# Performance work log

Hardware: AMD Instinct MI355X
Metric: run time of the kernel (lower is better)

The kernel has to match this reference:

```python
import jax, jax.numpy as jnp
import numpy as np

N_NODES = 30000
NEG_SLOPE = 0.2  # PyG GATConv default leaky_relu slope


def gat_conv(x, src, dst, W, a_src, a_dst, b, num_nodes, concat):
    """One PyG-style GATConv layer (add_self_loops already applied to src/dst).
    x: [N, F_in]; W: [F_in, H*C]; a_src, a_dst: [H, C]; b: [H*C] or [C].
    """
    H, C = a_src.shape
    h = (x @ W).reshape(num_nodes, H, C)                     # [N, H, C]
    alpha_src = jnp.einsum('nhc,hc->nh', h, a_src)           # [N, H]
    alpha_dst = jnp.einsum('nhc,hc->nh', h, a_dst)           # [N, H]
    e = jax.nn.leaky_relu(alpha_src[src] + alpha_dst[dst], NEG_SLOPE)  # [E, H]
    # scatter-softmax over incoming edges of each dst node
    e_max = jax.ops.segment_max(e, dst, num_segments=num_nodes)        # [N, H]
    e_exp = jnp.exp(e - e_max[dst])                                    # [E, H]
    denom = jax.ops.segment_sum(e_exp, dst, num_segments=num_nodes)    # [N, H]
    alpha = e_exp / denom[dst]                                         # [E, H]
    msg = h[src] * alpha[:, :, None]                                   # [E, H, C]
    out = jax.ops.segment_sum(msg, dst, num_segments=num_nodes)        # [N, H, C]
    out = out.reshape(num_nodes, H * C) if concat else out.mean(axis=1)
    return out + b


def _glorot(key, shape):
    fan = sum(shape[:2]) if len(shape) > 1 else shape[0] * 2
    return jax.random.normal(key, shape, dtype=jnp.float32) * np.sqrt(2.0 / fan)


def setup_inputs() -> dict:
    key = jax.random.key(0)
    ks = jax.random.split(key, 16)
    n, f_in, heads = N_NODES, 256, 4
    x = jax.random.normal(ks[0], (n, f_in), dtype=jnp.float32)
    edge_index = jax.random.randint(ks[1], (2, 480000), 0, n, dtype=jnp.int64)
    inp = {
        'x': x, 'edge_index': edge_index,
        'W1': _glorot(ks[2], (f_in, heads * 128)),
        'a1s': _glorot(ks[3], (heads, 128)), 'a1d': _glorot(ks[4], (heads, 128)),
        'b1': jnp.zeros((heads * 128,), jnp.float32),
        'W2': _glorot(ks[5], (heads * 128, heads * 128)),
        'a2s': _glorot(ks[6], (heads, 128)), 'a2d': _glorot(ks[7], (heads, 128)),
        'b2': jnp.zeros((heads * 128,), jnp.float32),
        'W3': _glorot(ks[8], (heads * 128, heads * 64)),
        'a3s': _glorot(ks[9], (heads, 64)), 'a3d': _glorot(ks[10], (heads, 64)),
        'b3': jnp.zeros((heads * 64,), jnp.float32),
        # conv4: 256 -> 64, 1 head, mean (concat=False)
        'W4': _glorot(ks[11], (heads * 64, 64)),
        'a4s': _glorot(ks[12], (1, 64)), 'a4d': _glorot(ks[13], (1, 64)),
        'b4': jnp.zeros((64,), jnp.float32),
    }
    return inp


def reference(x, edge_index, W1, a1s, a1d, b1, W2, a2s, a2d, b2,
              W3, a3s, a3d, b3, W4, a4s, a4d, b4):
    n = x.shape[0]
    # PyG GATConv default add_self_loops=True
    loops = jnp.arange(n, dtype=edge_index.dtype)
    src = jnp.concatenate([edge_index[0], loops])
    dst = jnp.concatenate([edge_index[1], loops])
    h = jax.nn.relu(gat_conv(x, src, dst, W1, a1s, a1d, b1, n, True))
    h = jax.nn.relu(gat_conv(h, src, dst, W2, a2s, a2d, b2, n, True))
    h = jax.nn.relu(gat_conv(h, src, dst, W3, a3s, a3d, b3, n, True))
    h = jax.nn.relu(gat_conv(h, src, dst, W4, a4s, a4d, b4, n, False))
    return h
```

## Files before the change

### kernel.cpp

```cpp
#include <hip/hip_runtime.h>
#include <hip/hip_fp16.h>
#include <math.h>


typedef __attribute__((ext_vector_type(8))) __bf16 bf16x8;
typedef __attribute__((ext_vector_type(4))) float floatx4;
typedef __attribute__((ext_vector_type(8))) unsigned short usv8;
typedef __attribute__((ext_vector_type(4))) unsigned short usv4;

#define DEG_CAP 256

__device__ __forceinline__ unsigned short f2bf(float f) {
    unsigned int u = __float_as_uint(f);
    u += 0x7fff + ((u >> 16) & 1);
    return (unsigned short)(u >> 16);
}
__device__ __forceinline__ float bf2f(unsigned short u) {
    return __uint_as_float(((unsigned int)u) << 16);
}
__device__ __forceinline__ float lrelu(float e) {
    return (e > 0.f) ? e : 0.2f * e;
}
__device__ __forceinline__ void gload16(const void* g, void* l) {
    __builtin_amdgcn_global_load_lds(
        (const __attribute__((address_space(1))) void*)g,
        (__attribute__((address_space(3))) void*)l, 16, 0, 0);
}

static __global__ void zero_float(float* __restrict__ p, int n) {
    int i = blockIdx.x * blockDim.x + threadIdx.x;
    if (i < n) p[i] = 0.f;
}
static __global__ void zero_int(int* __restrict__ p, int n) {
    int i = blockIdx.x * blockDim.x + threadIdx.x;
    if (i < n) p[i] = 0;
}

static __global__ void hist_kernel(const int* __restrict__ ei, int e0, int n_nodes,
                                   int* __restrict__ counts) {
    int e = blockIdx.x * blockDim.x + threadIdx.x;
    int et = e0 + n_nodes;
    if (e >= et) return;
    int d = (e < e0) ? ei[e0 + e] : (e - e0);
    atomicAdd(&counts[d], 1);
}

static __global__ void scan_kernel(const int* __restrict__ counts,
                                   int* __restrict__ row_ptr,
                                   int* __restrict__ cursor, int n) {
    __shared__ int sdata[1024];
    int tid = threadIdx.x;
    int per = (n + 1023) / 1024;
    int start = tid * per;
    int stop = min(start + per, n);
    if (start > n) start = n;
    int s = 0;
    for (int i = start; i < stop; i++) s += counts[i];
    sdata[tid] = s;
    __syncthreads();
    for (int off = 1; off < 1024; off <<= 1) {
        int t = (tid >= off) ? sdata[tid - off] : 0;
        __syncthreads();
        sdata[tid] += t;
        __syncthreads();
    }
    int run = sdata[tid] - s;
    for (int i = start; i < stop; i++) {
        row_ptr[i] = run;
        cursor[i] = run;
        run += counts[i];
    }
    if (stop == n) row_ptr[n] = run;
}

static __global__ void scatter_kernel(const int* __restrict__ ei, int e0, int n_nodes,
                                      int* __restrict__ cursor,
                                      int* __restrict__ src_sorted) {
    int e = blockIdx.x * blockDim.x + threadIdx.x;
    int et = e0 + n_nodes;
    if (e >= et) return;
    int s, d;
    if (e < e0) { s = ei[e]; d = ei[e0 + e]; } else { s = e - e0; d = s; }
    int pos = atomicAdd(&cursor[d], 1);
    src_sorted[pos] = s;
}

static __global__ void convA_kernel(const float* __restrict__ X,
                                    unsigned short* __restrict__ A, int M, int K) {
    int idx = blockIdx.x * 256 + threadIdx.x;
    if (idx >= M * K) return;
    int m = idx / K, k = idx % K;
    float v = X[idx];
    unsigned short hi = f2bf(v);
    size_t base = (size_t)m * (2 * K);
    A[base + k] = hi;
    A[base + K + k] = f2bf(v - bf2f(hi));
}

__device__ __forceinline__ void convW_one(const float* W, unsigned short* BT,
                                          int idx, int K, int N) {
    int n = idx / K, k = idx % K;
    float v = (n < N) ? W[(size_t)k * N + n] : 0.f;
    unsigned short hi = f2bf(v);
    size_t base = (size_t)n * (2 * K);
    BT[base + k] = hi;
    BT[base + K + k] = f2bf(v - bf2f(hi));
}

static __global__ void convW_all(const float* __restrict__ W1, unsigned short* __restrict__ BT1,
                                 const float* __restrict__ W2, unsigned short* __restrict__ BT2,
                                 const float* __restrict__ W3, unsigned short* __restrict__ BT3,
                                 const float* __restrict__ W4, unsigned short* __restrict__ BT4) {
    int idx = blockIdx.x * 256 + threadIdx.x;
    if (idx < 131072) { convW_one(W1, BT1, idx, 256, 512); return; }
    idx -= 131072;
    if (idx < 262144) { convW_one(W2, BT2, idx, 512, 512); return; }
    idx -= 262144;
    if (idx < 131072) { convW_one(W3, BT3, idx, 512, 256); return; }
    idx -= 131072;
    if (idx < 32768)  { convW_one(W4, BT4, idx, 256, 64); }
}

#define BM 128
#define BN 128
#define BKK 32

__launch_bounds__(256, 3)
static __global__ void gemm_mfma(const unsigned short* __restrict__ A,
                                 const unsigned short* __restrict__ B,
                                 __half* __restrict__ C, int M, int K, int N,
                                 int xcols, int mblocks,
                                 const float* __restrict__ asv,
                                 const float* __restrict__ adv,
                                 float* __restrict__ as_out,
                                 float* __restrict__ ad_out,
                                 int Hh, int Cc) {
    __shared__ __align__(16) unsigned short lds[4 * BM * BKK];
    const int tid  = threadIdx.x;
    const int lane = tid & 63;
    const int wave = tid >> 6;

    const int id = blockIdx.x;
    const int band = id / (8 * xcols);
    const int rem = id - band * 8 * xcols;
    const int band_rows = min(8, mblocks - band * 8);
    const int ry = rem % band_rows;
    const int rx = rem / band_rows;
    const int r0 = (band * 8 + ry) * BM;
    const int c0 = rx * BN;

    const int wm = (wave >> 1) * 64;
    const int wn = (wave & 1) * 64;
    const int q   = lane >> 4;
    const int m16 = lane & 15;

    floatx4 acc[4][4];
#pragma unroll
    for (int i = 0; i < 4; i++)
#pragma unroll
        for (int j = 0; j < 4; j++) acc[i][j] = {0.f, 0.f, 0.f, 0.f};

    const size_t sA = (size_t)(2 * K);
    const size_t sB = (size_t)(2 * K);
    char* ldsb = (char*)lds;

#pragma unroll 1
    for (int k0 = 0; k0 < K; k0 += BKK) {
        __syncthreads();
#pragma unroll
        for (int c = 0; c < 2; c++) {
            int slot = c * 256 + tid;
            int row = slot >> 2;
            int gc  = (slot & 3) ^ ((row >> 1) & 3);
            const unsigned short* Ab = A + (size_t)(r0 + row) * sA + k0 + gc * 8;
            const unsigned short* Bb = B + (size_t)(c0 + row) * sB + k0 + gc * 8;
            gload16(Ab,     ldsb + slot * 16);
            gload16(Ab + K, ldsb + 8192 + slot * 16);
            gload16(Bb,     ldsb + 16384 + slot * 16);
            gload16(Bb + K, ldsb + 24576 + slot * 16);
        }
        __syncthreads();
        bf16x8 ah[4], al[4], bh[4], bl[4];
#pragma unroll
        for (int i = 0; i < 4; i++) {
            int row = wm + i * 16 + m16;
            int ch  = q ^ ((row >> 1) & 3);
            int off = (row * 4 + ch) * 16;
            ah[i] = *(const bf16x8*)(ldsb + off);
            al[i] = *(const bf16x8*)(ldsb + 8192 + off);
        }
#pragma unroll
        for (int j = 0; j < 4; j++) {
            int row = wn + j * 16 + m16;
            int ch  = q ^ ((row >> 1) & 3);
            int off = (row * 4 + ch) * 16;
            bh[j] = *(const bf16x8*)(ldsb + 16384 + off);
            bl[j] = *(const bf16x8*)(ldsb + 24576 + off);
        }
#pragma unroll
        for (int i = 0; i < 4; i++)
#pragma unroll
            for (int j = 0; j < 4; j++) {
                acc[i][j] = __builtin_amdgcn_mfma_f32_16x16x32_bf16(
                    ah[i], bh[j], acc[i][j], 0, 0, 0);
                acc[i][j] = __builtin_amdgcn_mfma_f32_16x16x32_bf16(
                    al[i], bh[j], acc[i][j], 0, 0, 0);
                acc[i][j] = __builtin_amdgcn_mfma_f32_16x16x32_bf16(
                    ah[i], bl[j], acc[i][j], 0, 0, 0);
            }
    }
#pragma unroll
    for (int i = 0; i < 4; i++)
#pragma unroll
        for (int j = 0; j < 4; j++)
#pragma unroll
            for (int r = 0; r < 4; r++) {
                int row = r0 + wm + i * 16 + q * 4 + r;
                int col = c0 + wn + j * 16 + m16;
                if (row < M && col < N)
                    C[(size_t)row * N + col] = __float2half(acc[i][j][r]);
            }
    if (c0 + wn < N) {
        int head = (c0 + wn) / Cc;
#pragma unroll
        for (int i = 0; i < 4; i++)
#pragma unroll
            for (int r = 0; r < 4; r++) {
                float ps = 0.f, pd = 0.f;
#pragma unroll
                for (int j = 0; j < 4; j++) {
                    int c = c0 + wn + j * 16 + m16;
                    float v = acc[i][j][r];
                    ps = fmaf(v, asv[c], ps);
                    pd = fmaf(v, adv[c], pd);
                }
#pragma unroll
                for (int off = 1; off < 16; off <<= 1) {
                    ps += __shfl_xor(ps, off);
                    pd += __shfl_xor(pd, off);
                }
                if (m16 == 0) {
                    int row = r0 + wm + i * 16 + q * 4 + r;
                    if (row < M) {
                        atomicAdd(&as_out[(size_t)row * Hh + head], ps);
                        atomicAdd(&ad_out[(size_t)row * Hh + head], pd);
                    }
                }
            }
    }
}

template <int R>
__device__ __forceinline__ void accum_row(const __half* hptr, size_t off, float w,
                                          float* acc) {
    const __half* p = hptr + off;
    if constexpr (R == 8) {
        float4 raw = *(const float4*)p;
        const __half* hv = (const __half*)&raw;
#pragma unroll
        for (int r = 0; r < 8; r++) acc[r] = fmaf(__half2float(hv[r]), w, acc[r]);
    } else if constexpr (R == 4) {
        float2 raw = *(const float2*)p;
        const __half* hv = (const __half*)&raw;
#pragma unroll
        for (int r = 0; r < 4; r++) acc[r] = fmaf(__half2float(hv[r]), w, acc[r]);
    } else {
        acc[0] = fmaf(__half2float(*p), w, acc[0]);
    }
}

template <int H, int C, bool BF16OUT>
__launch_bounds__(256)
static __global__ void agg_kernel(const __half* __restrict__ h,
                                  const float* __restrict__ as_arr,
                                  const float* __restrict__ ad_arr,
                                  const int* __restrict__ row_ptr,
                                  const int* __restrict__ src_sorted,
                                  const float* __restrict__ bias,
                                  float* __restrict__ outf,
                                  unsigned short* __restrict__ outb,
                                  float* __restrict__ znext_as,
                                  float* __restrict__ znext_ad, int n_nodes) {
    constexpr int R = H * C / 64;
    constexpr int G = 64 / H;
    constexpr int K = H * C;
    __shared__ float lds_e[4][DEG_CAP * H];
    __shared__ int   lds_s[4][DEG_CAP];
    int wave = threadIdx.x >> 6;
    int lane = threadIdx.x & 63;
    int n = blockIdx.x * 4 + wave;
    if (n >= n_nodes) return;
    int beg = row_ptr[n], end = row_ptr[n + 1];
    float* we = lds_e[wave];
    int*   ls = lds_s[wave];

    float ad_h[H], m_h[H], l_h[H];
#pragma unroll
    for (int hh = 0; hh < H; hh++) {
        ad_h[hh] = ad_arr[(size_t)n * H + hh];
        m_h[hh] = -INFINITY;
        l_h[hh] = 0.f;
    }
    for (int base = beg; base < end; base += 64) {
        int j = base + lane;
        bool ok = j < end;
        float e_h[H];
        if (ok) {
            int s = src_sorted[j];
            if constexpr (H == 4) {
                float4 a = ((const float4*)as_arr)[s];
                e_h[0] = lrelu(a.x + ad_h[0]);
                e_h[1] = lrelu(a.y + ad_h[1]);
                e_h[2] = lrelu(a.z + ad_h[2]);
                e_h[3] = lrelu(a.w + ad_h[3]);
            } else {
                e_h[0] = lrelu(as_arr[s] + ad_h[0]);
            }
            int idx = j - beg;
            if (idx < DEG_CAP) {
                ls[idx] = s;
                if constexpr (H == 4) {
                    *(float4*)&we[idx * 4] = make_float4(e_h[0], e_h[1], e_h[2], e_h[3]);
                } else {
                    we[idx] = e_h[0];
                }
            }
        } else {
#pragma unroll
            for (int hh = 0; hh < H; hh++) e_h[hh] = -INFINITY;
        }
#pragma unroll
        for (int hh = 0; hh < H; hh++) {
            float cm = e_h[hh];
#pragma unroll
            for (int off = 1; off < 64; off <<= 1) cm = fmaxf(cm, __shfl_xor(cm, off));
            float newm = fmaxf(m_h[hh], cm);
            float p = ok ? __expf(e_h[hh] - newm) : 0.f;
#pragma unroll
            for (int off = 1; off < 64; off <<= 1) p += __shfl_xor(p, off);
            l_h[hh] = l_h[hh] * __expf(m_h[hh] - newm) + p;
            m_h[hh] = newm;
        }
    }
    int myh = lane / G;
    float mm, adm, inv;
    if constexpr (H == 4) {
        mm  = m_h[0];  mm  = (myh == 1) ? m_h[1] : mm;  mm  = (myh == 2) ? m_h[2] : mm;  mm  = (myh == 3) ? m_h[3] : mm;
        float ll = l_h[0]; ll = (myh == 1) ? l_h[1] : ll; ll = (myh == 2) ? l_h[2] : ll; ll = (myh == 3) ? l_h[3] : ll;
        adm = ad_h[0]; adm = (myh == 1) ? ad_h[1] : adm; adm = (myh == 2) ? ad_h[2] : adm; adm = (myh == 3) ? ad_h[3] : adm;
        inv = 1.f / ll;
    } else {
        mm = m_h[0]; adm = ad_h[0]; inv = 1.f / l_h[0];
    }

    float acc[R];
#pragma unroll
    for (int r = 0; r < R; r++) acc[r] = 0.f;

    int j = beg;
    for (; j + 7 < end; j += 8) {
        int i0 = j - beg;
        int ss[8];
        float ee[8];
        if (i0 + 7 < DEG_CAP) {
#pragma unroll
            for (int u = 0; u < 8; u++) {
                ss[u] = ls[i0 + u];
                ee[u] = we[(i0 + u) * H + myh];
            }
        } else {
#pragma unroll
            for (int u = 0; u < 8; u++) {
                ss[u] = src_sorted[j + u];
                ee[u] = lrelu(as_arr[(size_t)ss[u] * H + myh] + adm);
            }
        }
        float ww[8];
#pragma unroll
        for (int u = 0; u < 8; u++) ww[u] = __expf(ee[u] - mm) * inv;
#pragma unroll
        for (int u = 0; u < 8; u++)
            accum_row<R>(h, (size_t)ss[u] * K + lane * R, ww[u], acc);
    }
    for (; j < end; j++) {
        int i0 = j - beg;
        int s0;
        float e0;
        if (i0 < DEG_CAP) {
            s0 = ls[i0];
            e0 = we[i0 * H + myh];
        } else {
            s0 = src_sorted[j];
            e0 = lrelu(as_arr[(size_t)s0 * H + myh] + adm);
        }
        float w0 = __expf(e0 - mm) * inv;
        accum_row<R>(h, (size_t)s0 * K + lane * R, w0, acc);
    }

    if (znext_as != nullptr && lane == 0) {
        if constexpr (H == 4) {
            *(float4*)&znext_as[(size_t)n * 4] = make_float4(0.f, 0.f, 0.f, 0.f);
            *(float4*)&znext_ad[(size_t)n * 4] = make_float4(0.f, 0.f, 0.f, 0.f);
        } else {
            znext_as[n] = 0.f;
            znext_ad[n] = 0.f;
        }
    }
    float vout[R];
#pragma unroll
    for (int r = 0; r < R; r++)
        vout[r] = fmaxf(acc[r] + bias[lane * R + r], 0.f);

    if constexpr (BF16OUT) {
        unsigned short hi[R], lo[R];
#pragma unroll
        for (int r = 0; r < R; r++) {
            hi[r] = f2bf(vout[r]);
            lo[r] = f2bf(vout[r] - bf2f(hi[r]));
        }
        size_t base = (size_t)n * (2 * K) + lane * R;
        if constexpr (R == 8) {
            usv8 vh = {hi[0], hi[1], hi[2], hi[3], hi[4], hi[5], hi[6], hi[7]};
            usv8 vl = {lo[0], lo[1], lo[2], lo[3], lo[4], lo[5], lo[6], lo[7]};
            *(usv8*)(outb + base) = vh;
            *(usv8*)(outb + base + K) = vl;
        } else if constexpr (R == 4) {
            usv4 vh = {hi[0], hi[1], hi[2], hi[3]};
            usv4 vl = {lo[0], lo[1], lo[2], lo[3]};
            *(usv4*)(outb + base) = vh;
            *(usv4*)(outb + base + K) = vl;
        } else {
#pragma unroll
            for (int r = 0; r < R; r++) {
                outb[base + r] = hi[r];
                outb[base + K + r] = lo[r];
            }
        }
    } else {
#pragma unroll
        for (int r = 0; r < R; r++)
            outf[(size_t)n * K + lane * R + r] = vout[r];
    }
}


static inline size_t align_up(size_t x) { return (x + 255) & ~(size_t)255; }

extern "C" void kernel_launch(void* const* d_in, const int* in_sizes, int n_in,
                              void* d_out, int out_size, void* d_ws, size_t ws_size,
                              hipStream_t stream) {
    const float* x   = (const float*)d_in[0];
    const int*   ei  = (const int*)d_in[1];
    const float* W1  = (const float*)d_in[2];
    const float* a1s = (const float*)d_in[3];
    const float* a1d = (const float*)d_in[4];
    const float* b1  = (const float*)d_in[5];
    const float* W2  = (const float*)d_in[6];
    const float* a2s = (const float*)d_in[7];
    const float* a2d = (const float*)d_in[8];
    const float* b2  = (const float*)d_in[9];
    const float* W3  = (const float*)d_in[10];
    const float* a3s = (const float*)d_in[11];
    const float* a3d = (const float*)d_in[12];
    const float* b3  = (const float*)d_in[13];
    const float* W4  = (const float*)d_in[14];
    const float* a4s = (const float*)d_in[15];
    const float* a4d = (const float*)d_in[16];
    const float* b4  = (const float*)d_in[17];

    const int n  = in_sizes[0] / 256;
    const int e0 = in_sizes[1] / 2;
    const int et = e0 + n;
    const int Mpad = ((n + 127) / 128) * 128;

    char* w = (char*)d_ws;
    unsigned short* slotA = (unsigned short*)w;  w += align_up((size_t)Mpad * 1024 * 2);
    __half* hbuf = (__half*)w;                   w += align_up((size_t)n * 512 * 4);
    unsigned short* WT1 = (unsigned short*)w;    w += align_up((size_t)512 * 512 * 2);
    unsigned short* WT2 = (unsigned short*)w;    w += align_up((size_t)512 * 1024 * 2);
    unsigned short* WT3 = (unsigned short*)w;    w += align_up((size_t)256 * 1024 * 2);
    unsigned short* WT4 = (unsigned short*)w;    w += align_up((size_t)128 * 512 * 2);
    float* asA = (float*)w;                      w += align_up((size_t)n * 4 * 4);
    float* adA = (float*)w;                      w += align_up((size_t)n * 4 * 4);
    float* asB = (float*)w;                      w += align_up((size_t)n * 4 * 4);
    float* adB = (float*)w;                      w += align_up((size_t)n * 4 * 4);
    int* row_ptr = (int*)w;                      w += align_up((size_t)(n + 1) * 4);
    int* counts  = (int*)w;                      w += align_up((size_t)n * 4);
    int* cursor  = (int*)w;                      w += align_up((size_t)n * 4);
    int* src_sorted = (int*)w;                   w += align_up((size_t)et * 4);
    (void)ws_size;

    dim3 blk(256);
    int nodeblocks = (n + 3) / 4;

    zero_int<<<(n + 255) / 256, 256, 0, stream>>>(counts, n);
    hist_kernel<<<(et + 255) / 256, 256, 0, stream>>>(ei, e0, n, counts);
    scan_kernel<<<1, 1024, 0, stream>>>(counts, row_ptr, cursor, n);
    scatter_kernel<<<(et + 255) / 256, 256, 0, stream>>>(ei, e0, n, cursor, src_sorted);

    convA_kernel<<<((n * 256) + 255) / 256, blk, 0, stream>>>(x, slotA, n, 256);
    convW_all<<<(557056 + 255) / 256, blk, 0, stream>>>(W1, WT1, W2, WT2, W3, WT3, W4, WT4);
    zero_float<<<(n * 8 + 255) / 256, blk, 0, stream>>>(asA, n * 8);

    const int mblocks = Mpad / 128;

    gemm_mfma<<<dim3(4 * mblocks), blk, 0, stream>>>(slotA, WT1, hbuf, n, 256, 512, 4, mblocks,
                                                     a1s, a1d, asA, adA, 4, 128);
    agg_kernel<4, 128, true><<<nodeblocks, blk, 0, stream>>>(hbuf, asA, adA, row_ptr, src_sorted, b1, nullptr, slotA, asB, adB, n);

    gemm_mfma<<<dim3(4 * mblocks), blk, 0, stream>>>(slotA, WT2, hbuf, n, 512, 512, 4, mblocks,
                                                     a2s, a2d, asB, adB, 4, 128);
    agg_kernel<4, 128, true><<<nodeblocks, blk, 0, stream>>>(hbuf, asB, adB, row_ptr, src_sorted, b2, nullptr, slotA, asA, adA, n);

    gemm_mfma<<<dim3(2 * mblocks), blk, 0, stream>>>(slotA, WT3, hbuf, n, 512, 256, 2, mblocks,
                                                     a3s, a3d, asA, adA, 4, 64);
    agg_kernel<4, 64, true><<<nodeblocks, blk, 0, stream>>>(hbuf, asA, adA, row_ptr, src_sorted, b3, nullptr, slotA, asB, adB, n);

    gemm_mfma<<<dim3(1 * mblocks), blk, 0, stream>>>(slotA, WT4, hbuf, n, 256, 64, 1, mblocks,
                                                     a4s, a4d, asB, adB, 1, 64);
    agg_kernel<1, 64, false><<<nodeblocks, blk, 0, stream>>>(hbuf, asB, adB, row_ptr, src_sorted, b4, (float*)d_out, nullptr, nullptr, nullptr, n);
}
```

Baseline: 646.0 us.

## Split GAT aggregation into edge-weight pass and column-sliced gather kernel

Splits each multi-head aggregation into two kernels. A per-node softmax kernel writes normalized edge weights to a global buffer. A sliced aggregation kernel then assigns each wave one node and a 64-column slice, so many more blocks run in parallel. The goal is more parallelism and lower register pressure in the gather. In exchange it adds kernel launches, a round trip of edge weights through global memory, repeated index reads per slice, and narrower 2-byte gathers instead of 16-byte vector loads. The last layer gets a dedicated single-head kernel.

New measurement: 860.9 us. 1.33x slower.

```diff
diff --git a/kernel.cpp b/kernel.cpp
--- a/kernel.cpp
+++ b/kernel.cpp
@@ -5,8 +5,6 @@
 
 typedef __attribute__((ext_vector_type(8))) __bf16 bf16x8;
 typedef __attribute__((ext_vector_type(4))) float floatx4;
-typedef __attribute__((ext_vector_type(8))) unsigned short usv8;
-typedef __attribute__((ext_vector_type(4))) unsigned short usv4;
 
 #define DEG_CAP 256
 
@@ -250,49 +248,22 @@
     }
 }
 
-template <int R>
-__device__ __forceinline__ void accum_row(const __half* hptr, size_t off, float w,
-                                          float* acc) {
-    const __half* p = hptr + off;
-    if constexpr (R == 8) {
-        float4 raw = *(const float4*)p;
-        const __half* hv = (const __half*)&raw;
-#pragma unroll
-        for (int r = 0; r < 8; r++) acc[r] = fmaf(__half2float(hv[r]), w, acc[r]);
-    } else if constexpr (R == 4) {
-        float2 raw = *(const float2*)p;
-        const __half* hv = (const __half*)&raw;
-#pragma unroll
-        for (int r = 0; r < 4; r++) acc[r] = fmaf(__half2float(hv[r]), w, acc[r]);
-    } else {
-        acc[0] = fmaf(__half2float(*p), w, acc[0]);
-    }
-}
-
-template <int H, int C, bool BF16OUT>
+template <int H>
 __launch_bounds__(256)
-static __global__ void agg_kernel(const __half* __restrict__ h,
-                                  const float* __restrict__ as_arr,
-                                  const float* __restrict__ ad_arr,
-                                  const int* __restrict__ row_ptr,
-                                  const int* __restrict__ src_sorted,
-                                  const float* __restrict__ bias,
-                                  float* __restrict__ outf,
-                                  unsigned short* __restrict__ outb,
-                                  float* __restrict__ znext_as,
-                                  float* __restrict__ znext_ad, int n_nodes) {
-    constexpr int R = H * C / 64;
-    constexpr int G = 64 / H;
-    constexpr int K = H * C;
+static __global__ void weight_kernel(const float* __restrict__ as_arr,
+                                     const float* __restrict__ ad_arr,
+                                     const int* __restrict__ row_ptr,
+                                     const int* __restrict__ src_sorted,
+                                     float* __restrict__ wout, int E_tot,
+                                     float* __restrict__ znext_as,
+                                     float* __restrict__ znext_ad, int n_nodes) {
     __shared__ float lds_e[4][DEG_CAP * H];
-    __shared__ int   lds_s[4][DEG_CAP];
     int wave = threadIdx.x >> 6;
     int lane = threadIdx.x & 63;
     int n = blockIdx.x * 4 + wave;
     if (n >= n_nodes) return;
     int beg = row_ptr[n], end = row_ptr[n + 1];
     float* we = lds_e[wave];
-    int*   ls = lds_s[wave];
 
     float ad_h[H], m_h[H], l_h[H];
 #pragma unroll
@@ -318,7 +289,6 @@
             }
             int idx = j - beg;
             if (idx < DEG_CAP) {
-                ls[idx] = s;
                 if constexpr (H == 4) {
                     *(float4*)&we[idx * 4] = make_float4(e_h[0], e_h[1], e_h[2], e_h[3]);
                 } else {
@@ -342,105 +312,172 @@
             m_h[hh] = newm;
         }
     }
-    int myh = lane / G;
-    float mm, adm, inv;
-    if constexpr (H == 4) {
-        mm  = m_h[0];  mm  = (myh == 1) ? m_h[1] : mm;  mm  = (myh == 2) ? m_h[2] : mm;  mm  = (myh == 3) ? m_h[3] : mm;
-        float ll = l_h[0]; ll = (myh == 1) ? l_h[1] : ll; ll = (myh == 2) ? l_h[2] : ll; ll = (myh == 3) ? l_h[3] : ll;
-        adm = ad_h[0]; adm = (myh == 1) ? ad_h[1] : adm; adm = (myh == 2) ? ad_h[2] : adm; adm = (myh == 3) ? ad_h[3] : adm;
-        inv = 1.f / ll;
-    } else {
-        mm = m_h[0]; adm = ad_h[0]; inv = 1.f / l_h[0];
-    }
-
-    float acc[R];
-#pragma unroll
-    for (int r = 0; r < R; r++) acc[r] = 0.f;
-
+    float inv_h[H];
+#pragma unroll
+    for (int hh = 0; hh < H; hh++) inv_h[hh] = 1.f / l_h[hh];
+
+    if (znext_as != nullptr && lane == 0) {
+        *(float4*)&znext_as[(size_t)n * 4] = make_float4(0.f, 0.f, 0.f, 0.f);
+        *(float4*)&znext_ad[(size_t)n * 4] = make_float4(0.f, 0.f, 0.f, 0.f);
+    }
+
+    for (int base = beg; base < end; base += 64) {
+        int j = base + lane;
+        if (j < end) {
+            int idx = j - beg;
+            float e_h[H];
+            if (idx < DEG_CAP) {
+                if constexpr (H == 4) {
+                    float4 t = *(const float4*)&we[idx * 4];
+                    e_h[0] = t.x; e_h[1] = t.y; e_h[2] = t.z; e_h[3] = t.w;
+                } else {
+                    e_h[0] = we[idx];
+                }
+            } else {
+                int s = src_sorted[j];
+                if constexpr (H == 4) {
+                    float4 a = ((const float4*)as_arr)[s];
+                    e_h[0] = lrelu(a.x + ad_h[0]);
+                    e_h[1] = lrelu(a.y + ad_h[1]);
+                    e_h[2] = lrelu(a.z + ad_h[2]);
+                    e_h[3] = lrelu(a.w + ad_h[3]);
+                } else {
+                    e_h[0] = lrelu(as_arr[s] + ad_h[0]);
+                }
+            }
+#pragma unroll
+            for (int hh = 0; hh < H; hh++)
+                wout[(size_t)hh * E_tot + j] = __expf(e_h[hh] - m_h[hh]) * inv_h[hh];
+        }
+    }
+}
+
+template <int H, int C, bool BF16OUT>
+__launch_bounds__(256)
+static __global__ void slice_agg(const __half* __restrict__ h,
+                                 const float* __restrict__ wbuf,
+                                 const int* __restrict__ row_ptr,
+                                 const int* __restrict__ src_sorted,
+                                 const float* __restrict__ bias,
+                                 float* __restrict__ outf,
+                                 unsigned short* __restrict__ outb,
+                                 int E_tot, int n_nodes) {
+    constexpr int K = H * C;
+    constexpr int NS = K / 64;
+    int id = blockIdx.x;
+    int nb = id / NS;
+    int slice = id - nb * NS;
+    int wave = threadIdx.x >> 6;
+    int lane = threadIdx.x & 63;
+    int n = nb * 4 + wave;
+    if (n >= n_nodes) return;
+    int col = slice * 64 + lane;
+    int head = (slice * 64) / C;
+    const float* wh = wbuf + (size_t)head * E_tot;
+    int beg = row_ptr[n], end = row_ptr[n + 1];
+
+    float acc = 0.f;
     int j = beg;
     for (; j + 7 < end; j += 8) {
+        int ss[8];
+        float wg[8];
+#pragma unroll
+        for (int u = 0; u < 8; u++) ss[u] = src_sorted[j + u];
+#pragma unroll
+        for (int u = 0; u < 8; u++) wg[u] = wh[j + u];
+        __half hv[8];
+#pragma unroll
+        for (int u = 0; u < 8; u++) hv[u] = h[(size_t)ss[u] * K + col];
+#pragma unroll
+        for (int u = 0; u < 8; u++) acc = fmaf(__half2float(hv[u]), wg[u], acc);
+    }
+    for (; j < end; j++) {
+        int s = src_sorted[j];
+        float wg = wh[j];
+        acc = fmaf(__half2float(h[(size_t)s * K + col]), wg, acc);
+    }
+
+    float v = fmaxf(acc + bias[col], 0.f);
+    if constexpr (BF16OUT) {
+        unsigned short hi = f2bf(v);
+        unsigned short lo = f2bf(v - bf2f(hi));
+        size_t base = (size_t)n * (2 * K) + col;
+        outb[base] = hi;
+        outb[base + K] = lo;
+    } else {
+        outf[(size_t)n * K + col] = v;
+    }
+}
+
+__launch_bounds__(256)
+static __global__ void agg4_kernel(const __half* __restrict__ h,
+                                   const float* __restrict__ as_arr,
+                                   const float* __restrict__ ad_arr,
+                                   const int* __restrict__ row_ptr,
+                                   const int* __restrict__ src_sorted,
+                                   const float* __restrict__ bias,
+                                   float* __restrict__ outf, int n_nodes) {
+    __shared__ float lds_e[4][DEG_CAP];
+    int wave = threadIdx.x >> 6;
+    int lane = threadIdx.x & 63;
+    int n = blockIdx.x * 4 + wave;
+    if (n >= n_nodes) return;
+    int beg = row_ptr[n], end = row_ptr[n + 1];
+    float* we = lds_e[wave];
+
+    float ad_n = ad_arr[n];
+    float m = -INFINITY, l = 0.f;
+    for (int base = beg; base < end; base += 64) {
+        int j = base + lane;
+        bool ok = j < end;
+        float e = -INFINITY;
+        if (ok) {
+            int s = src_sorted[j];
+            e = lrelu(as_arr[s] + ad_n);
+            int idx = j - beg;
+            if (idx < DEG_CAP) we[idx] = e;
+        }
+        float cm = e;
+#pragma unroll
+        for (int off = 1; off < 64; off <<= 1) cm = fmaxf(cm, __shfl_xor(cm, off));
+        float newm = fmaxf(m, cm);
+        float p = ok ? __expf(e - newm) : 0.f;
+#pragma unroll
+        for (int off = 1; off < 64; off <<= 1) p += __shfl_xor(p, off);
+        l = l * __expf(m - newm) + p;
+        m = newm;
+    }
+    float inv = 1.f / l;
+
+    float acc = 0.f;
+    int j = beg;
+    for (; j + 3 < end; j += 4) {
         int i0 = j - beg;
-        int ss[8];
-        float ee[8];
-        if (i0 + 7 < DEG_CAP) {
-#pragma unroll
-            for (int u = 0; u < 8; u++) {
-                ss[u] = ls[i0 + u];
-                ee[u] = we[(i0 + u) * H + myh];
-            }
+        int ss[4];
+        float ee[4];
+#pragma unroll
+        for (int u = 0; u < 4; u++) ss[u] = src_sorted[j + u];
+        if (i0 + 3 < DEG_CAP) {
+#pragma unroll
+            for (int u = 0; u < 4; u++) ee[u] = we[i0 + u];
         } else {
 #pragma unroll
-            for (int u = 0; u < 8; u++) {
-                ss[u] = src_sorted[j + u];
-                ee[u] = lrelu(as_arr[(size_t)ss[u] * H + myh] + adm);
-            }
-        }
-        float ww[8];
-#pragma unroll
-        for (int u = 0; u < 8; u++) ww[u] = __expf(ee[u] - mm) * inv;
-#pragma unroll
-        for (int u = 0; u < 8; u++)
-            accum_row<R>(h, (size_t)ss[u] * K + lane * R, ww[u], acc);
+            for (int u = 0; u < 4; u++) ee[u] = lrelu(as_arr[ss[u]] + ad_n);
+        }
+        __half hv[4];
+#pragma unroll
+        for (int u = 0; u < 4; u++) hv[u] = h[(size_t)ss[u] * 64 + lane];
+#pragma unroll
+        for (int u = 0; u < 4; u++)
+            acc = fmaf(__half2float(hv[u]), __expf(ee[u] - m) * inv, acc);
     }
     for (; j < end; j++) {
         int i0 = j - beg;
-        int s0;
-        float e0;
-        if (i0 < DEG_CAP) {
-            s0 = ls[i0];
-            e0 = we[i0 * H + myh];
-        } else {
-            s0 = src_sorted[j];
-            e0 = lrelu(as_arr[(size_t)s0 * H + myh] + adm);
-        }
-        float w0 = __expf(e0 - mm) * inv;
-        accum_row<R>(h, (size_t)s0 * K + lane * R, w0, acc);
-    }
-
-    if (znext_as != nullptr && lane == 0) {
-        if constexpr (H == 4) {
-            *(float4*)&znext_as[(size_t)n * 4] = make_float4(0.f, 0.f, 0.f, 0.f);
-            *(float4*)&znext_ad[(size_t)n * 4] = make_float4(0.f, 0.f, 0.f, 0.f);
-        } else {
-            znext_as[n] = 0.f;
-            znext_ad[n] = 0.f;
-        }
-    }
-    float vout[R];
-#pragma unroll
-    for (int r = 0; r < R; r++)
-        vout[r] = fmaxf(acc[r] + bias[lane * R + r], 0.f);
-
-    if constexpr (BF16OUT) {
-        unsigned short hi[R], lo[R];
-#pragma unroll
-        for (int r = 0; r < R; r++) {
-            hi[r] = f2bf(vout[r]);
-            lo[r] = f2bf(vout[r] - bf2f(hi[r]));
-        }
-        size_t base = (size_t)n * (2 * K) + lane * R;
-        if constexpr (R == 8) {
-            usv8 vh = {hi[0], hi[1], hi[2], hi[3], hi[4], hi[5], hi[6], hi[7]};
-            usv8 vl = {lo[0], lo[1], lo[2], lo[3], lo[4], lo[5], lo[6], lo[7]};
-            *(usv8*)(outb + base) = vh;
-            *(usv8*)(outb + base + K) = vl;
-        } else if constexpr (R == 4) {
-            usv4 vh = {hi[0], hi[1], hi[2], hi[3]};
-            usv4 vl = {lo[0], lo[1], lo[2], lo[3]};
-            *(usv4*)(outb + base) = vh;
-            *(usv4*)(outb + base + K) = vl;
-        } else {
-#pragma unroll
-            for (int r = 0; r < R; r++) {
-                outb[base + r] = hi[r];
-                outb[base + K + r] = lo[r];
-            }
-        }
-    } else {
-#pragma unroll
-        for (int r = 0; r < R; r++)
-            outf[(size_t)n * K + lane * R + r] = vout[r];
-    }
+        int s = src_sorted[j];
+        float e = (i0 < DEG_CAP) ? we[i0] : lrelu(as_arr[s] + ad_n);
+        acc = fmaf(__half2float(h[(size_t)s * 64 + lane]), __expf(e - m) * inv, acc);
+    }
+    outf[(size_t)n * 64 + lane] = fmaxf(acc + bias[lane], 0.f);
 }
 
 
@@ -475,7 +512,8 @@
 
     char* w = (char*)d_ws;
     unsigned short* slotA = (unsigned short*)w;  w += align_up((size_t)Mpad * 1024 * 2);
-    __half* hbuf = (__half*)w;                   w += align_up((size_t)n * 512 * 4);
+    __half* hbuf = (__half*)w;                   w += align_up((size_t)n * 512 * 2);
+    float* wbuf = (float*)w;                     w += align_up((size_t)4 * et * 4);
     unsigned short* WT1 = (unsigned short*)w;    w += align_up((size_t)512 * 512 * 2);
     unsigned short* WT2 = (unsigned short*)w;    w += align_up((size_t)512 * 1024 * 2);
     unsigned short* WT3 = (unsigned short*)w;    w += align_up((size_t)256 * 1024 * 2);
@@ -506,17 +544,20 @@
 
     gemm_mfma<<<dim3(4 * mblocks), blk, 0, stream>>>(slotA, WT1, hbuf, n, 256, 512, 4, mblocks,
                                                      a1s, a1d, asA, adA, 4, 128);
-    agg_kernel<4, 128, true><<<nodeblocks, blk, 0, stream>>>(hbuf, asA, adA, row_ptr, src_sorted, b1, nullptr, slotA, asB, adB, n);
+    weight_kernel<4><<<nodeblocks, blk, 0, stream>>>(asA, adA, row_ptr, src_sorted, wbuf, et, asB, adB, n);
+    slice_agg<4, 128, true><<<dim3(nodeblocks * 8), blk, 0, stream>>>(hbuf, wbuf, row_ptr, src_sorted, b1, nullptr, slotA, et, n);
 
     gemm_mfma<<<dim3(4 * mblocks), blk, 0, stream>>>(slotA, WT2, hbuf, n, 512, 512, 4, mblocks,
                                                      a2s, a2d, asB, adB, 4, 128);
-    agg_kernel<4, 128, true><<<nodeblocks, blk, 0, stream>>>(hbuf, asB, adB, row_ptr, src_sorted, b2, nullptr, slotA, asA, adA, n);
+    weight_kernel<4><<<nodeblocks, blk, 0, stream>>>(asB, adB, row_ptr, src_sorted, wbuf, et, asA, adA, n);
+    slice_agg<4, 128, true><<<dim3(nodeblocks * 8), blk, 0, stream>>>(hbuf, wbuf, row_ptr, src_sorted, b2, nullptr, slotA, et, n);
 
     gemm_mfma<<<dim3(2 * mblocks), blk, 0, stream>>>(slotA, WT3, hbuf, n, 512, 256, 2, mblocks,
                                                      a3s, a3d, asA, adA, 4, 64);
-    agg_kernel<4, 64, true><<<nodeblocks, blk, 0, stream>>>(hbuf, asA, adA, row_ptr, src_sorted, b3, nullptr, slotA, asB, adB, n);
+    weight_kernel<4><<<nodeblocks, blk, 0, stream>>>(asA, adA, row_ptr, src_sorted, wbuf, et, asB, adB, n);
+    slice_agg<4, 64, true><<<dim3(nodeblocks * 4), blk, 0, stream>>>(hbuf, wbuf, row_ptr, src_sorted, b3, nullptr, slotA, et, n);
 
     gemm_mfma<<<dim3(1 * mblocks), blk, 0, stream>>>(slotA, WT4, hbuf, n, 256, 64, 1, mblocks,
                                                      a4s, a4d, asB, adB, 1, 64);
-    agg_kernel<1, 64, false><<<nodeblocks, blk, 0, stream>>>(hbuf, asB, adB, row_ptr, src_sorted, b4, (float*)d_out, nullptr, nullptr, nullptr, n);
-}
+    agg4_kernel<<<nodeblocks, blk, 0, stream>>>(hbuf, asB, adB, row_ptr, src_sorted, b4, (float*)d_out, n);
+}
```
